# Kernel tuning notes

Measured on AMD Instinct MI355X. Metric: run time of the kernel, lower is better.

Reference implementation:

```python
import jax, jax.numpy as jnp
import numpy as np

B, V, H = 128, 50257, 2048   # batch, vocab, history length
NEG_INF = jnp.float32(-jnp.inf)
TEMP_MIN = 1e-5


def setup_inputs() -> dict:
    key = jax.random.key(0)
    k1, k2, k3 = jax.random.split(key, 3)
    logits = jax.random.normal(k1, (B, V), jnp.float32) * 4.0
    previous_tokens = jax.random.randint(k2, (B, H), 0, V)
    # uniform noise for the exponential-race (Gumbel-max) draw; strictly positive
    u = jax.random.uniform(k3, (B, V), jnp.float32, minval=1e-10, maxval=1.0)
    return {
        "logits": logits,
        "previous_tokens": previous_tokens,
        "u": u,
        "top_p": jnp.full((1,), 0.9, jnp.float32),
        "repetition_penalty": jnp.full((1,), 1.35, jnp.float32),
        "temperature": jnp.full((1,), 0.7, jnp.float32),
        "top_k": 50,
    }


def _logits_to_probs(logits, previous_tokens, temperature, top_k, top_p, repetition_penalty):
    b = jnp.arange(logits.shape[0])[:, None]  # [B,1] row index for scatters
    # repetition penalty: gather history scores, shrink, scatter back
    score = jnp.take_along_axis(logits, previous_tokens, axis=1)          # [B,H]
    score = jnp.where(score < 0, score * repetition_penalty, score / repetition_penalty)
    logits = logits.at[b, previous_tokens].set(score)                     # [B,V]
    # nucleus (top-p) filtering via descending sort + cumulative softmax
    order = jnp.argsort(-logits, axis=-1)                                 # [B,V]
    sorted_logits = jnp.take_along_axis(logits, order, axis=1)
    cum_probs = jnp.cumsum(jax.nn.softmax(sorted_logits, axis=-1), axis=-1)
    remove_sorted = cum_probs > top_p
    remove_sorted = remove_sorted.at[:, 0].set(False)                     # keep best token
    # scatter removal mask back to vocab order (order is a permutation)
    remove = jnp.zeros_like(remove_sorted).at[b, order].set(remove_sorted)
    logits = jnp.where(remove, NEG_INF, logits)
    # temperature + top-k pivot filter
    logits = logits / jnp.maximum(temperature, TEMP_MIN)
    v = jax.lax.top_k(logits, top_k)[0]                                   # [B,top_k]
    pivot = v[:, -1:]
    logits = jnp.where(logits < pivot, NEG_INF, logits)
    return jax.nn.softmax(logits, axis=-1)


def reference(logits, previous_tokens, u, top_p, repetition_penalty, temperature, top_k):
    previous_tokens = previous_tokens.astype(jnp.int32)
    probs = _logits_to_probs(logits, previous_tokens, temperature, top_k, top_p,
                             repetition_penalty)
    # multinomial_sample_one_no_sync: exponential race argmax(probs / Exp(1))
    q = -jnp.log(u)
    idx_next = jnp.argmax(probs / q, axis=-1, keepdims=True).astype(jnp.int32)
    return idx_next, probs
```

## Files before the change

kernel.cpp:

```cpp
#include <hip/hip_runtime.h>
#include <cfloat>
#include <cmath>
#include <cstdint>

#define VV 50257
#define SPLITS 4
#define CHUNKA 12568
#define BMW ((CHUNKA + 31) / 32)
#define NBUCK 4096
#define CAPC 256
#define K1T 512
#define K2T 512
#define NJ 7
#define NW1 (K1T / 64)

__device__ __forceinline__ unsigned fmono(float f) {
    unsigned b = __float_as_uint(f);
    return b ^ (((int)b < 0) ? 0xFFFFFFFFu : 0x80000000u);
}
__device__ __forceinline__ float unmono(unsigned m) {
    unsigned b = (m & 0x80000000u) ? (m ^ 0x80000000u) : ~m;
    return __uint_as_float(b);
}
__device__ __forceinline__ uint64_t mkkey(unsigned mono, int idx) {
    return ((uint64_t)mono << 32) | (unsigned)(~idx);
}

__global__ __launch_bounds__(K1T) void pp_k1(
    const float* __restrict__ logits, const int* __restrict__ prev,
    const float* __restrict__ rpp,
    float* __restrict__ pm, float* __restrict__ ps,
    uint64_t* __restrict__ gkey, int* __restrict__ gcnt,
    float* __restrict__ out_probs, int Hp, int capc)
{
    const int sp = blockIdx.x, row = blockIdx.y;
    const int tid = threadIdx.x, lane = tid & 63, wid = tid >> 6;
    const int c0 = sp * CHUNKA;
    const int c1 = min(VV, c0 + CHUNKA);
    const int len = c1 - c0;
    const float rp = rpp[0], inv_rp = 1.0f / rp;

    __shared__ unsigned bm[BMW];
    __shared__ unsigned hist[NBUCK];
    __shared__ float red_m[NW1], red_s[NW1];
    __shared__ unsigned wtot[NW1];
    __shared__ uint64_t cand_k[CAPC];
    __shared__ float sM;
    __shared__ int sT, sCnt;

    for (int i = tid; i < BMW; i += K1T) bm[i] = 0u;
    for (int i = tid; i < NBUCK; i += K1T) hist[i] = 0u;
    if (tid == 0) { sT = 0; sCnt = 0; }
    __syncthreads();

    const int* prow = prev + (size_t)row * Hp;
    for (int i = tid; i < Hp; i += K1T) {
        int t = prow[i];
        if (t >= c0 && t < c1) {
            int o = t - c0;
            atomicOr(&bm[o >> 5], 1u << (o & 31));
        }
    }
    __syncthreads();

    const float* lrow = logits + (size_t)row * VV;
    float* orow = out_probs + (size_t)row * VV;
    const int pad = (4 - (row & 3)) & 3;
    const int n4 = (len - pad) >> 2;
    const int tail0 = pad + 4 * n4;
    const float4* l4 = (const float4*)(lrow + c0 + pad);
    float4* o4 = (float4*)(orow + c0 + pad);

    float4 rv[NJ];
    float m = -FLT_MAX;
    for (int o = tid; o < pad; o += K1T) {
        float l = lrow[c0 + o];
        if ((bm[o >> 5] >> (o & 31)) & 1u) l = (l < 0.f) ? l * rp : l * inv_rp;
        atomicAdd(&hist[fmono(l) >> 20], 1u);
        m = fmaxf(m, l);
    }
    #pragma unroll
    for (int j = 0; j < NJ; ++j) {
        int k = tid + j * K1T;
        if (k < n4) {
            float4 v = l4[k];
            int ob = pad + 4 * k;
            float x;
            x = v.x; if ((bm[(ob+0) >> 5] >> ((ob+0) & 31)) & 1u) x = (x < 0.f) ? x * rp : x * inv_rp;
            atomicAdd(&hist[fmono(x) >> 20], 1u); m = fmaxf(m, x); v.x = x;
            x = v.y; if ((bm[(ob+1) >> 5] >> ((ob+1) & 31)) & 1u) x = (x < 0.f) ? x * rp : x * inv_rp;
            atomicAdd(&hist[fmono(x) >> 20], 1u); m = fmaxf(m, x); v.y = x;
            x = v.z; if ((bm[(ob+2) >> 5] >> ((ob+2) & 31)) & 1u) x = (x < 0.f) ? x * rp : x * inv_rp;
            atomicAdd(&hist[fmono(x) >> 20], 1u); m = fmaxf(m, x); v.z = x;
            x = v.w; if ((bm[(ob+3) >> 5] >> ((ob+3) & 31)) & 1u) x = (x < 0.f) ? x * rp : x * inv_rp;
            atomicAdd(&hist[fmono(x) >> 20], 1u); m = fmaxf(m, x); v.w = x;
            rv[j] = v;
        }
    }
    for (int o = tail0 + tid; o < len; o += K1T) {
        float l = lrow[c0 + o];
        if ((bm[o >> 5] >> (o & 31)) & 1u) l = (l < 0.f) ? l * rp : l * inv_rp;
        atomicAdd(&hist[fmono(l) >> 20], 1u);
        m = fmaxf(m, l);
    }

    for (int o = tid; o < pad; o += K1T) orow[c0 + o] = 0.f;
    const float4 z4 = make_float4(0.f, 0.f, 0.f, 0.f);
    for (int k = tid; k < n4; k += K1T) o4[k] = z4;
    for (int o = tail0 + tid; o < len; o += K1T) orow[c0 + o] = 0.f;

    #pragma unroll
    for (int off = 32; off; off >>= 1) m = fmaxf(m, __shfl_down(m, off));
    if (lane == 0) red_m[wid] = m;
    __syncthreads();
    if (tid == 0) {
        float M = red_m[0];
        for (int w = 1; w < NW1; ++w) M = fmaxf(M, red_m[w]);
        sM = M;
    }

    unsigned c = 0;
    #pragma unroll
    for (int j = 0; j < 8; ++j) c += hist[tid * 8 + j];
    unsigned v = c;
    #pragma unroll
    for (int off = 1; off < 64; off <<= 1) {
        unsigned o = __shfl_down(v, off);
        if (lane + off < 64) v += o;
    }
    if (lane == 0) wtot[wid] = v;
    __syncthreads();
    unsigned add = 0;
    for (int w = wid + 1; w < NW1; ++w) add += wtot[w];
    const unsigned mySuf = v + add;
    const unsigned sufExcl = mySuf - c;
    if (mySuf >= 64u && sufExcl < 64u) {
        unsigned above = sufExcl;
        for (int b = tid * 8 + 7; b >= tid * 8; --b) {
            above += hist[b];
            if (above >= 64u) { sT = b; break; }
        }
    }
    __syncthreads();
    const unsigned T = (unsigned)sT;
    const float M = sM;
    const int cmax = min(capc, CAPC);

    float s = 0.0f;
    for (int o = tid; o < pad; o += K1T) {
        float l = lrow[c0 + o];
        if ((bm[o >> 5] >> (o & 31)) & 1u) l = (l < 0.f) ? l * rp : l * inv_rp;
        s += __expf(l - M);
        unsigned mo = fmono(l);
        if ((mo >> 20) >= T) {
            int p = atomicAdd(&sCnt, 1);
            if (p < cmax) cand_k[p] = mkkey(mo, c0 + o);
        }
    }
    #pragma unroll
    for (int j = 0; j < NJ; ++j) {
        int k = tid + j * K1T;
        if (k < n4) {
            float4 vv = rv[j];
            int gi = c0 + pad + 4 * k;
            unsigned mo;
            s += __expf(vv.x - M);
            mo = fmono(vv.x);
            if ((mo >> 20) >= T) { int p = atomicAdd(&sCnt, 1); if (p < cmax) cand_k[p] = mkkey(mo, gi + 0); }
            s += __expf(vv.y - M);
            mo = fmono(vv.y);
            if ((mo >> 20) >= T) { int p = atomicAdd(&sCnt, 1); if (p < cmax) cand_k[p] = mkkey(mo, gi + 1); }
            s += __expf(vv.z - M);
            mo = fmono(vv.z);
            if ((mo >> 20) >= T) { int p = atomicAdd(&sCnt, 1); if (p < cmax) cand_k[p] = mkkey(mo, gi + 2); }
            s += __expf(vv.w - M);
            mo = fmono(vv.w);
            if ((mo >> 20) >= T) { int p = atomicAdd(&sCnt, 1); if (p < cmax) cand_k[p] = mkkey(mo, gi + 3); }
        }
    }
    for (int o = tail0 + tid; o < len; o += K1T) {
        float l = lrow[c0 + o];
        if ((bm[o >> 5] >> (o & 31)) & 1u) l = (l < 0.f) ? l * rp : l * inv_rp;
        s += __expf(l - M);
        unsigned mo = fmono(l);
        if ((mo >> 20) >= T) {
            int p = atomicAdd(&sCnt, 1);
            if (p < cmax) cand_k[p] = mkkey(mo, c0 + o);
        }
    }
    #pragma unroll
    for (int off = 32; off; off >>= 1) s += __shfl_down(s, off);
    if (lane == 0) red_s[wid] = s;
    __syncthreads();

    const int slot = row * SPLITS + sp;
    if (tid == 0) {
        float Ss = red_s[0];
        for (int w = 1; w < NW1; ++w) Ss += red_s[w];
        pm[slot] = M;
        ps[slot] = Ss;
        gcnt[slot] = min(sCnt, cmax);
    }
    const int cnt = min(sCnt, cmax);
    for (int t = tid; t < cnt; t += K1T)
        gkey[(size_t)slot * capc + t] = cand_k[t];
}

__global__ __launch_bounds__(K2T) void pp_k2(
    const float* __restrict__ u, const float* __restrict__ toppp,
    const float* __restrict__ tempp, const int* __restrict__ topkp,
    const float* __restrict__ pm, const float* __restrict__ ps,
    const uint64_t* __restrict__ gkey, const int* __restrict__ gcnt,
    float* __restrict__ out_idx, float* __restrict__ out_probs, int capc)
{
    const int row = blockIdx.x, tid = threadIdx.x;
    __shared__ uint64_t ck[SPLITS * CAPC];
    __shared__ uint64_t tk[64];
    __shared__ float sM, sS;

    int c4[SPLITS], off[SPLITS];
    int tot = 0;
    #pragma unroll
    for (int j = 0; j < SPLITS; ++j) {
        c4[j] = gcnt[row * SPLITS + j];
        off[j] = tot;
        tot += c4[j];
    }
    #pragma unroll
    for (int j = 0; j < SPLITS; ++j)
        for (int i = tid; i < c4[j]; i += K2T)
            ck[off[j] + i] = gkey[(size_t)(row * SPLITS + j) * capc + i];
    if (tid < 64) tk[tid] = 0ull;
    if (tid == 0) {
        float M = pm[row * SPLITS], S = ps[row * SPLITS];
        for (int j = 1; j < SPLITS; ++j) {
            float m2 = pm[row * SPLITS + j], s2 = ps[row * SPLITS + j];
            float nm = fmaxf(M, m2);
            S = S * __expf(M - nm) + s2 * __expf(m2 - nm);
            M = nm;
        }
        sM = M; sS = S;
    }
    __syncthreads();

    for (int t = tid; t < tot; t += K2T) {
        const uint64_t ki = ck[t];
        int r = 0;
        int j = 0;
        for (; j + 8 <= tot; j += 8) {
            uint64_t a0 = ck[j], a1 = ck[j+1], a2 = ck[j+2], a3 = ck[j+3];
            uint64_t a4 = ck[j+4], a5 = ck[j+5], a6 = ck[j+6], a7 = ck[j+7];
            r += (int)(a0 > ki) + (int)(a1 > ki) + (int)(a2 > ki) + (int)(a3 > ki)
               + (int)(a4 > ki) + (int)(a5 > ki) + (int)(a6 > ki) + (int)(a7 > ki);
        }
        for (; j < tot; ++j) r += (int)(ck[j] > ki);
        if (r < 64) tk[r] = ki;
    }
    __syncthreads();

    if (tid < 64) {
        const int lane = tid;
        const float top_p = toppp[0];
        const float temp = tempp[0];
        int K = topkp[0]; K = min(max(K, 1), 64);
        const float M = sM, Ssum = sS;
        uint64_t k64 = tk[lane];
        bool val = (lane < min(tot, 64));
        float vl = unmono((unsigned)(k64 >> 32));
        int ci = (int)(~(unsigned)(k64 & 0xFFFFFFFFu));
        bool act = (lane < K) && val;
        float e = act ? expf(vl - M) / Ssum : 0.0f;
        float cum = e;
        #pragma unroll
        for (int off2 = 1; off2 < 64; off2 <<= 1) {
            float pv = __shfl_up(cum, off2);
            if (lane >= off2) cum += pv;
        }
        unsigned long long bal = __ballot(act && (cum <= top_p));
        int n = (int)__popcll(bal);
        if (n < 1) n = 1;
        const float v0 = __shfl(vl, 0);
        const float invT = 1.0f / fmaxf(temp, 1e-5f);
        bool keep = (lane < n) && val;
        float w = keep ? expf((vl - v0) * invT) : 0.0f;
        float Z = w;
        #pragma unroll
        for (int off2 = 32; off2; off2 >>= 1) Z += __shfl_xor(Z, off2);
        float p = keep ? (w / Z) : 0.0f;
        if (keep) out_probs[(size_t)row * VV + ci] = p;
        float ratio = -1.0f;
        if (keep) ratio = p / (-logf(u[(size_t)row * VV + ci]));
        int bi = keep ? ci : 0x7FFFFFFF;
        #pragma unroll
        for (int off2 = 32; off2; off2 >>= 1) {
            float orat = __shfl_xor(ratio, off2);
            int oidx = __shfl_xor(bi, off2);
            if (orat > ratio || (orat == ratio && oidx < bi)) { ratio = orat; bi = oidx; }
        }
        if (lane == 0) out_idx[row] = (float)bi;
    }
}

extern "C" void kernel_launch(void* const* d_in, const int* in_sizes, int n_in,
                              void* d_out, int out_size, void* d_ws, size_t ws_size,
                              hipStream_t stream) {
    const float* logits = (const float*)d_in[0];
    const int*   prev   = (const int*)d_in[1];
    const float* u      = (const float*)d_in[2];
    const float* topp   = (const float*)d_in[3];
    const float* rp     = (const float*)d_in[4];
    const float* temp   = (const float*)d_in[5];
    const int*   topk   = (const int*)d_in[6];

    const int B  = in_sizes[0] / VV;
    const int Hp = in_sizes[1] / B;

    char* ws = (char*)d_ws;
    int*   gcnt = (int*)ws;
    float* pm   = (float*)(ws + 8192);
    float* ps   = pm + (size_t)B * SPLITS;
    long long avail = (long long)ws_size - 16384;
    int capc = (int)(avail / (8LL * B * SPLITS));
    if (capc > CAPC) capc = CAPC;
    if (capc < 64) capc = 64;
    uint64_t* gkey = (uint64_t*)(ws + 16384);

    float* out = (float*)d_out;
    pp_k1<<<dim3(SPLITS, B), K1T, 0, stream>>>(
        logits, prev, rp, pm, ps, gkey, gcnt, out + B, Hp, capc);
    pp_k2<<<B, K2T, 0, stream>>>(
        u, topp, temp, topk, pm, ps, gkey, gcnt, out, out + B, capc);
}
```

Measured before the change: 32.47 us.

## Select per-split top-64 in stage one and merge sorted lists by binary search

Each split block now ranks its own candidates in shared memory and writes a sorted top-64 list, so the second kernel loads only 4x64 keys and ranks them by binary search across the other sorted lists, instead of running a quadratic rank over up to 1024 keys. Stage one also stops holding the logit tile in registers and rereads it from global memory in the second pass, targets 4 blocks per CU through launch bounds, vectorizes the history load with int4, and moves the zero-fill of the output to the end of the kernel. The trade-off is extra global reads and a quadratic rank step inside stage one. Validity checks for splits with fewer than 64 candidates are dropped, which assumes every split always yields at least 64.

```diff
diff --git a/kernel.cpp b/kernel.cpp
--- a/kernel.cpp
+++ b/kernel.cpp
@@ -8,10 +8,9 @@
 #define CHUNKA 12568
 #define BMW ((CHUNKA + 31) / 32)
 #define NBUCK 4096
-#define CAPC 256
+#define CAPC 512
 #define K1T 512
-#define K2T 512
-#define NJ 7
+#define K2T 256
 #define NW1 (K1T / 64)
 
 __device__ __forceinline__ unsigned fmono(float f) {
@@ -26,12 +25,11 @@
     return ((uint64_t)mono << 32) | (unsigned)(~idx);
 }
 
-__global__ __launch_bounds__(K1T) void pp_k1(
+__global__ __launch_bounds__(K1T, 4) void pp_k1(
     const float* __restrict__ logits, const int* __restrict__ prev,
     const float* __restrict__ rpp,
     float* __restrict__ pm, float* __restrict__ ps,
-    uint64_t* __restrict__ gkey, int* __restrict__ gcnt,
-    float* __restrict__ out_probs, int Hp, int capc)
+    uint64_t* __restrict__ gkey, float* __restrict__ out_probs, int Hp)
 {
     const int sp = blockIdx.x, row = blockIdx.y;
     const int tid = threadIdx.x, lane = tid & 63, wid = tid >> 6;
@@ -45,6 +43,7 @@
     __shared__ float red_m[NW1], red_s[NW1];
     __shared__ unsigned wtot[NW1];
     __shared__ uint64_t cand_k[CAPC];
+    __shared__ uint64_t top64[64];
     __shared__ float sM;
     __shared__ int sT, sCnt;
 
@@ -54,12 +53,19 @@
     __syncthreads();
 
     const int* prow = prev + (size_t)row * Hp;
-    for (int i = tid; i < Hp; i += K1T) {
+    const int h4 = Hp >> 2;
+    const int4* prow4 = (const int4*)prow;
+    for (int i = tid; i < h4; i += K1T) {
+        int4 t4 = prow4[i];
+        int t;
+        t = t4.x; if (t >= c0 && t < c1) { int o = t - c0; atomicOr(&bm[o >> 5], 1u << (o & 31)); }
+        t = t4.y; if (t >= c0 && t < c1) { int o = t - c0; atomicOr(&bm[o >> 5], 1u << (o & 31)); }
+        t = t4.z; if (t >= c0 && t < c1) { int o = t - c0; atomicOr(&bm[o >> 5], 1u << (o & 31)); }
+        t = t4.w; if (t >= c0 && t < c1) { int o = t - c0; atomicOr(&bm[o >> 5], 1u << (o & 31)); }
+    }
+    for (int i = 4 * h4 + tid; i < Hp; i += K1T) {
         int t = prow[i];
-        if (t >= c0 && t < c1) {
-            int o = t - c0;
-            atomicOr(&bm[o >> 5], 1u << (o & 31));
-        }
+        if (t >= c0 && t < c1) { int o = t - c0; atomicOr(&bm[o >> 5], 1u << (o & 31)); }
     }
     __syncthreads();
 
@@ -71,7 +77,6 @@
     const float4* l4 = (const float4*)(lrow + c0 + pad);
     float4* o4 = (float4*)(orow + c0 + pad);
 
-    float4 rv[NJ];
     float m = -FLT_MAX;
     for (int o = tid; o < pad; o += K1T) {
         float l = lrow[c0 + o];
@@ -79,23 +84,19 @@
         atomicAdd(&hist[fmono(l) >> 20], 1u);
         m = fmaxf(m, l);
     }
-    #pragma unroll
-    for (int j = 0; j < NJ; ++j) {
-        int k = tid + j * K1T;
-        if (k < n4) {
-            float4 v = l4[k];
-            int ob = pad + 4 * k;
-            float x;
-            x = v.x; if ((bm[(ob+0) >> 5] >> ((ob+0) & 31)) & 1u) x = (x < 0.f) ? x * rp : x * inv_rp;
-            atomicAdd(&hist[fmono(x) >> 20], 1u); m = fmaxf(m, x); v.x = x;
-            x = v.y; if ((bm[(ob+1) >> 5] >> ((ob+1) & 31)) & 1u) x = (x < 0.f) ? x * rp : x * inv_rp;
-            atomicAdd(&hist[fmono(x) >> 20], 1u); m = fmaxf(m, x); v.y = x;
-            x = v.z; if ((bm[(ob+2) >> 5] >> ((ob+2) & 31)) & 1u) x = (x < 0.f) ? x * rp : x * inv_rp;
-            atomicAdd(&hist[fmono(x) >> 20], 1u); m = fmaxf(m, x); v.z = x;
-            x = v.w; if ((bm[(ob+3) >> 5] >> ((ob+3) & 31)) & 1u) x = (x < 0.f) ? x * rp : x * inv_rp;
-            atomicAdd(&hist[fmono(x) >> 20], 1u); m = fmaxf(m, x); v.w = x;
-            rv[j] = v;
-        }
+    #pragma unroll 4
+    for (int k = tid; k < n4; k += K1T) {
+        float4 v = l4[k];
+        const int ob = pad + 4 * k;
+        float x;
+        x = v.x; if ((bm[(ob+0) >> 5] >> ((ob+0) & 31)) & 1u) x = (x < 0.f) ? x * rp : x * inv_rp;
+        atomicAdd(&hist[fmono(x) >> 20], 1u); m = fmaxf(m, x);
+        x = v.y; if ((bm[(ob+1) >> 5] >> ((ob+1) & 31)) & 1u) x = (x < 0.f) ? x * rp : x * inv_rp;
+        atomicAdd(&hist[fmono(x) >> 20], 1u); m = fmaxf(m, x);
+        x = v.z; if ((bm[(ob+2) >> 5] >> ((ob+2) & 31)) & 1u) x = (x < 0.f) ? x * rp : x * inv_rp;
+        atomicAdd(&hist[fmono(x) >> 20], 1u); m = fmaxf(m, x);
+        x = v.w; if ((bm[(ob+3) >> 5] >> ((ob+3) & 31)) & 1u) x = (x < 0.f) ? x * rp : x * inv_rp;
+        atomicAdd(&hist[fmono(x) >> 20], 1u); m = fmaxf(m, x);
     }
     for (int o = tail0 + tid; o < len; o += K1T) {
         float l = lrow[c0 + o];
@@ -103,11 +104,6 @@
         atomicAdd(&hist[fmono(l) >> 20], 1u);
         m = fmaxf(m, l);
     }
-
-    for (int o = tid; o < pad; o += K1T) orow[c0 + o] = 0.f;
-    const float4 z4 = make_float4(0.f, 0.f, 0.f, 0.f);
-    for (int k = tid; k < n4; k += K1T) o4[k] = z4;
-    for (int o = tail0 + tid; o < len; o += K1T) orow[c0 + o] = 0.f;
 
     #pragma unroll
     for (int off = 32; off; off >>= 1) m = fmaxf(m, __shfl_down(m, off));
@@ -144,7 +140,6 @@
     __syncthreads();
     const unsigned T = (unsigned)sT;
     const float M = sM;
-    const int cmax = min(capc, CAPC);
 
     float s = 0.0f;
     for (int o = tid; o < pad; o += K1T) {
@@ -154,29 +149,27 @@
         unsigned mo = fmono(l);
         if ((mo >> 20) >= T) {
             int p = atomicAdd(&sCnt, 1);
-            if (p < cmax) cand_k[p] = mkkey(mo, c0 + o);
-        }
-    }
-    #pragma unroll
-    for (int j = 0; j < NJ; ++j) {
-        int k = tid + j * K1T;
-        if (k < n4) {
-            float4 vv = rv[j];
-            int gi = c0 + pad + 4 * k;
-            unsigned mo;
-            s += __expf(vv.x - M);
-            mo = fmono(vv.x);
-            if ((mo >> 20) >= T) { int p = atomicAdd(&sCnt, 1); if (p < cmax) cand_k[p] = mkkey(mo, gi + 0); }
-            s += __expf(vv.y - M);
-            mo = fmono(vv.y);
-            if ((mo >> 20) >= T) { int p = atomicAdd(&sCnt, 1); if (p < cmax) cand_k[p] = mkkey(mo, gi + 1); }
-            s += __expf(vv.z - M);
-            mo = fmono(vv.z);
-            if ((mo >> 20) >= T) { int p = atomicAdd(&sCnt, 1); if (p < cmax) cand_k[p] = mkkey(mo, gi + 2); }
-            s += __expf(vv.w - M);
-            mo = fmono(vv.w);
-            if ((mo >> 20) >= T) { int p = atomicAdd(&sCnt, 1); if (p < cmax) cand_k[p] = mkkey(mo, gi + 3); }
-        }
+            if (p < CAPC) cand_k[p] = mkkey(mo, c0 + o);
+        }
+    }
+    #pragma unroll 4
+    for (int k = tid; k < n4; k += K1T) {
+        float4 vv = l4[k];
+        const int gi = c0 + pad + 4 * k;
+        const int ob = pad + 4 * k;
+        float x; unsigned mo;
+        x = vv.x; if ((bm[(ob+0) >> 5] >> ((ob+0) & 31)) & 1u) x = (x < 0.f) ? x * rp : x * inv_rp;
+        s += __expf(x - M); mo = fmono(x);
+        if ((mo >> 20) >= T) { int p = atomicAdd(&sCnt, 1); if (p < CAPC) cand_k[p] = mkkey(mo, gi + 0); }
+        x = vv.y; if ((bm[(ob+1) >> 5] >> ((ob+1) & 31)) & 1u) x = (x < 0.f) ? x * rp : x * inv_rp;
+        s += __expf(x - M); mo = fmono(x);
+        if ((mo >> 20) >= T) { int p = atomicAdd(&sCnt, 1); if (p < CAPC) cand_k[p] = mkkey(mo, gi + 1); }
+        x = vv.z; if ((bm[(ob+2) >> 5] >> ((ob+2) & 31)) & 1u) x = (x < 0.f) ? x * rp : x * inv_rp;
+        s += __expf(x - M); mo = fmono(x);
+        if ((mo >> 20) >= T) { int p = atomicAdd(&sCnt, 1); if (p < CAPC) cand_k[p] = mkkey(mo, gi + 2); }
+        x = vv.w; if ((bm[(ob+3) >> 5] >> ((ob+3) & 31)) & 1u) x = (x < 0.f) ? x * rp : x * inv_rp;
+        s += __expf(x - M); mo = fmono(x);
+        if ((mo >> 20) >= T) { int p = atomicAdd(&sCnt, 1); if (p < CAPC) cand_k[p] = mkkey(mo, gi + 3); }
     }
     for (int o = tail0 + tid; o < len; o += K1T) {
         float l = lrow[c0 + o];
@@ -185,7 +178,7 @@
         unsigned mo = fmono(l);
         if ((mo >> 20) >= T) {
             int p = atomicAdd(&sCnt, 1);
-            if (p < cmax) cand_k[p] = mkkey(mo, c0 + o);
+            if (p < CAPC) cand_k[p] = mkkey(mo, c0 + o);
         }
     }
     #pragma unroll
@@ -199,38 +192,44 @@
         for (int w = 1; w < NW1; ++w) Ss += red_s[w];
         pm[slot] = M;
         ps[slot] = Ss;
-        gcnt[slot] = min(sCnt, cmax);
-    }
-    const int cnt = min(sCnt, cmax);
-    for (int t = tid; t < cnt; t += K1T)
-        gkey[(size_t)slot * capc + t] = cand_k[t];
+    }
+
+    const int cnt = min(sCnt, CAPC);
+    for (int t = tid; t < cnt; t += K1T) {
+        const uint64_t ki = cand_k[t];
+        int r = 0;
+        int j = 0;
+        for (; j + 8 <= cnt; j += 8) {
+            uint64_t a0 = cand_k[j],   a1 = cand_k[j+1], a2 = cand_k[j+2], a3 = cand_k[j+3];
+            uint64_t a4 = cand_k[j+4], a5 = cand_k[j+5], a6 = cand_k[j+6], a7 = cand_k[j+7];
+            r += (int)(a0 > ki) + (int)(a1 > ki) + (int)(a2 > ki) + (int)(a3 > ki)
+               + (int)(a4 > ki) + (int)(a5 > ki) + (int)(a6 > ki) + (int)(a7 > ki);
+        }
+        for (; j < cnt; ++j) r += (int)(cand_k[j] > ki);
+        if (r < 64) top64[r] = ki;
+    }
+    __syncthreads();
+    if (tid < 64) gkey[(size_t)slot * 64 + tid] = top64[tid];
+
+    for (int o = tid; o < pad; o += K1T) orow[c0 + o] = 0.f;
+    const float4 z4 = make_float4(0.f, 0.f, 0.f, 0.f);
+    for (int k = tid; k < n4; k += K1T) o4[k] = z4;
+    for (int o = tail0 + tid; o < len; o += K1T) orow[c0 + o] = 0.f;
 }
 
 __global__ __launch_bounds__(K2T) void pp_k2(
     const float* __restrict__ u, const float* __restrict__ toppp,
     const float* __restrict__ tempp, const int* __restrict__ topkp,
     const float* __restrict__ pm, const float* __restrict__ ps,
-    const uint64_t* __restrict__ gkey, const int* __restrict__ gcnt,
-    float* __restrict__ out_idx, float* __restrict__ out_probs, int capc)
+    const uint64_t* __restrict__ gkey,
+    float* __restrict__ out_idx, float* __restrict__ out_probs)
 {
     const int row = blockIdx.x, tid = threadIdx.x;
-    __shared__ uint64_t ck[SPLITS * CAPC];
+    __shared__ uint64_t ck[SPLITS * 64];
     __shared__ uint64_t tk[64];
     __shared__ float sM, sS;
 
-    int c4[SPLITS], off[SPLITS];
-    int tot = 0;
-    #pragma unroll
-    for (int j = 0; j < SPLITS; ++j) {
-        c4[j] = gcnt[row * SPLITS + j];
-        off[j] = tot;
-        tot += c4[j];
-    }
-    #pragma unroll
-    for (int j = 0; j < SPLITS; ++j)
-        for (int i = tid; i < c4[j]; i += K2T)
-            ck[off[j] + i] = gkey[(size_t)(row * SPLITS + j) * capc + i];
-    if (tid < 64) tk[tid] = 0ull;
+    ck[tid] = gkey[(size_t)row * (SPLITS * 64) + tid];
     if (tid == 0) {
         float M = pm[row * SPLITS], S = ps[row * SPLITS];
         for (int j = 1; j < SPLITS; ++j) {
@@ -243,17 +242,21 @@
     }
     __syncthreads();
 
-    for (int t = tid; t < tot; t += K2T) {
-        const uint64_t ki = ck[t];
-        int r = 0;
-        int j = 0;
-        for (; j + 8 <= tot; j += 8) {
-            uint64_t a0 = ck[j], a1 = ck[j+1], a2 = ck[j+2], a3 = ck[j+3];
-            uint64_t a4 = ck[j+4], a5 = ck[j+5], a6 = ck[j+6], a7 = ck[j+7];
-            r += (int)(a0 > ki) + (int)(a1 > ki) + (int)(a2 > ki) + (int)(a3 > ki)
-               + (int)(a4 > ki) + (int)(a5 > ki) + (int)(a6 > ki) + (int)(a7 > ki);
-        }
-        for (; j < tot; ++j) r += (int)(ck[j] > ki);
+    {
+        const int j = tid >> 6;
+        const uint64_t ki = ck[tid];
+        int r = tid & 63;
+        #pragma unroll
+        for (int o = 0; o < SPLITS; ++o) {
+            if (o == j) continue;
+            const uint64_t* ls = &ck[o * 64];
+            int lo = 0, hi = 64;
+            while (lo < hi) {
+                int mid = (lo + hi) >> 1;
+                if (ls[mid] > ki) lo = mid + 1; else hi = mid;
+            }
+            r += lo;
+        }
         if (r < 64) tk[r] = ki;
     }
     __syncthreads();
@@ -264,11 +267,10 @@
         const float temp = tempp[0];
         int K = topkp[0]; K = min(max(K, 1), 64);
         const float M = sM, Ssum = sS;
-        uint64_t k64 = tk[lane];
-        bool val = (lane < min(tot, 64));
-        float vl = unmono((unsigned)(k64 >> 32));
-        int ci = (int)(~(unsigned)(k64 & 0xFFFFFFFFu));
-        bool act = (lane < K) && val;
+        const uint64_t k64 = tk[lane];
+        const float vl = unmono((unsigned)(k64 >> 32));
+        const int ci = (int)(~(unsigned)(k64 & 0xFFFFFFFFu));
+        bool act = (lane < K);
         float e = act ? expf(vl - M) / Ssum : 0.0f;
         float cum = e;
         #pragma unroll
@@ -281,7 +283,7 @@
         if (n < 1) n = 1;
         const float v0 = __shfl(vl, 0);
         const float invT = 1.0f / fmaxf(temp, 1e-5f);
-        bool keep = (lane < n) && val;
+        bool keep = (lane < n);
         float w = keep ? expf((vl - v0) * invT) : 0.0f;
         float Z = w;
         #pragma unroll
@@ -316,18 +318,13 @@
     const int Hp = in_sizes[1] / B;
 
     char* ws = (char*)d_ws;
-    int*   gcnt = (int*)ws;
-    float* pm   = (float*)(ws + 8192);
-    float* ps   = pm + (size_t)B * SPLITS;
-    long long avail = (long long)ws_size - 16384;
-    int capc = (int)(avail / (8LL * B * SPLITS));
-    if (capc > CAPC) capc = CAPC;
-    if (capc < 64) capc = 64;
+    float* pm = (float*)ws;
+    float* ps = pm + (size_t)B * SPLITS;
     uint64_t* gkey = (uint64_t*)(ws + 16384);
 
     float* out = (float*)d_out;
     pp_k1<<<dim3(SPLITS, B), K1T, 0, stream>>>(
-        logits, prev, rp, pm, ps, gkey, gcnt, out + B, Hp, capc);
+        logits, prev, rp, pm, ps, gkey, out + B, Hp);
     pp_k2<<<B, K2T, 0, stream>>>(
-        u, topp, temp, topk, pm, ps, gkey, gcnt, out, out + B, capc);
-}
+        u, topp, temp, topk, pm, ps, gkey, out, out + B);
+}
```

Measured after the change: 29.39 us. -9.5%, faster.
